# Kernel optimization log

Measured on AMD Instinct MI355X. Metric: run time of the kernel, lower is better.

The kernel has to match this reference:

```python
import jax, jax.numpy as jnp
import numpy as np

BITS = 4
MAXQ = (1 << BITS) - 1  # 15
GROUPSIZE = 128
IN_F = 8192
OUT_F = 8192
PACK = 32 // BITS  # 8 values per int32


def setup_inputs() -> dict:
    key = jax.random.key(0)
    k_x, k_w, k_z, k_s, k_b = jax.random.split(key, 5)
    groups = IN_F // GROUPSIZE
    x = jax.random.normal(k_x, (4, 32, IN_F), dtype=jnp.float32)
    # bit-packed int32 weight / zeros (random bit patterns are valid quantized data)
    qweight = jax.random.randint(k_w, (IN_F // PACK, OUT_F), 0, 2**31 - 1, dtype=jnp.int32)
    qzeros = jax.random.randint(k_z, (groups, OUT_F // PACK), 0, 2**31 - 1, dtype=jnp.int32)
    scales = (jax.random.uniform(k_s, (groups, OUT_F), dtype=jnp.float32) * 0.01 + 1e-3)
    g_idx = (jnp.arange(IN_F, dtype=jnp.int32) // GROUPSIZE).astype(jnp.int32)
    bias = jax.random.normal(k_b, (OUT_F,), dtype=jnp.float32) * 0.01
    return {"x": x, "qweight": qweight, "qzeros": qzeros, "scales": scales,
            "g_idx": g_idx, "bias": bias}


def _dequant(qweight, qzeros, scales, g_idx):
    shifts = jnp.arange(0, 32, BITS, dtype=jnp.int32)  # [PACK]
    # unpack weights along the input dim: [in/PACK, PACK, out] -> [in, out]
    w = (qweight[:, None, :] >> shifts[None, :, None]) & MAXQ
    w = w.reshape(-1, qweight.shape[1])
    # unpack zeros along the output dim: [groups, out/PACK, PACK] -> [groups, out]
    # GPTQ stores (zero - 1), so add 1 back
    z = ((qzeros[:, :, None] >> shifts[None, None, :]) & MAXQ) + 1
    z = z.reshape(qzeros.shape[0], -1)
    # per-group dequant: W[i, o] = scales[g_idx[i], o] * (w[i, o] - z[g_idx[i], o])
    W = scales[g_idx] * (w.astype(scales.dtype) - z[g_idx].astype(scales.dtype))
    return W  # [in, out]


def reference(x, qweight, qzeros, scales, g_idx, bias):
    W = _dequant(qweight, qzeros, scales, g_idx)
    out = jnp.einsum('bsi,io->bso', x, W) + bias
    return out
```

## Files before the change

kernel.cpp:

```cpp
#include <hip/hip_runtime.h>
#include <hip/hip_bf16.h>
#include <stdint.h>


#define IN_F 8192
#define OUT_F 8192
#define MROWS 128
#define KSPLIT 8
#define KCHUNK 1024
#define BM 64

typedef short short8_t __attribute__((ext_vector_type(8)));
typedef float float4_t __attribute__((ext_vector_type(4)));
typedef float float16_t __attribute__((ext_vector_type(16)));

__device__ __forceinline__ void gl_lds16(const void* g, void* l) {
  auto g1 = (const __attribute__((address_space(1))) unsigned int*)((uintptr_t)g);
  auto l3 = (__attribute__((address_space(3))) unsigned int*)((uintptr_t)l);
  __builtin_amdgcn_global_load_lds(g1, l3, 16, 0, 0);
}

__global__ void cvt_x(const float* __restrict__ x, unsigned short* __restrict__ xb) {
  const int i = (blockIdx.x * 256 + threadIdx.x) * 8;
  float4_t a = *(const float4_t*)(x + i);
  float4_t b = *(const float4_t*)(x + i + 4);
  union { short8_t v; __hip_bfloat162 h[4]; } u;
  u.h[0] = __float22bfloat162_rn(make_float2(a.x, a.y));
  u.h[1] = __float22bfloat162_rn(make_float2(a.z, a.w));
  u.h[2] = __float22bfloat162_rn(make_float2(b.x, b.y));
  u.h[3] = __float22bfloat162_rn(make_float2(b.z, b.w));
  *(short8_t*)(xb + i) = u.v;
}

__global__ void reduce_out(const float* __restrict__ part, const float* __restrict__ bias,
                           float* __restrict__ out) {
  const int i = (blockIdx.x * 256 + threadIdx.x) * 4;
  const int o = i & (OUT_F - 1);
  float4_t s = *(const float4_t*)(bias + o);
#pragma unroll
  for (int sl = 0; sl < KSPLIT; ++sl)
    s += *(const float4_t*)(part + (size_t)sl * MROWS * OUT_F + i);
  *(float4_t*)(out + i) = s;
}

__global__ __launch_bounds__(512, 2) void gptq_gemm(
    const unsigned short* __restrict__ xb,
    const int* __restrict__ qweight,
    const int* __restrict__ qzeros,
    const float* __restrict__ scales,
    float* __restrict__ part)
{
  __shared__ unsigned short As[BM * KCHUNK];

  const int tid  = threadIdx.x;
  const int lane = tid & 63;
  const int l31  = lane & 31;
  const int half = lane >> 5;
  const int wv   = tid >> 6;

  const int bid = blockIdx.x;
  const int kb  = bid >> 5;
  const int mb  = (bid >> 4) & 1;
  const int nb  = bid & 15;

  const int kc0 = kb * KCHUNK;
  const int m0  = mb * BM;
  const int g0  = kc0 >> 7;
  const int kp_base = (kc0 >> 3) + half;

  int col[2];
  col[0] = nb * 512 + wv * 64 + l31;
  col[1] = col[0] + 32;

  int   qwc[8][2], qwn[8][2];
  float scc[2], scn[2];
  int   zqc[2], zqn[2];
#pragma unroll
  for (int ks = 0; ks < 8; ++ks)
#pragma unroll
    for (int nt = 0; nt < 2; ++nt)
      qwc[ks][nt] = qweight[(size_t)(kp_base + ks * 2) * OUT_F + col[nt]];
#pragma unroll
  for (int nt = 0; nt < 2; ++nt) {
    scc[nt] = scales[g0 * OUT_F + col[nt]];
    zqc[nt] = qzeros[g0 * (OUT_F / 8) + (col[nt] >> 3)];
  }

  for (int rq = 0; rq < 8; ++rq) {
    const int rl = wv * 8 + rq;
    const unsigned short* grow = xb + (size_t)(m0 + rl) * IN_F + kc0;
#pragma unroll
    for (int hf = 0; hf < 2; ++hf) {
      const int p = hf * 64 + lane;
      const int c = (p & 0x70) | ((p ^ (rl & 15)) & 15);
      gl_lds16(grow + c * 8, (void*)(As + ((size_t)rl * 128 + hf * 64) * 8));
    }
  }
  __syncthreads();

  float16_t acc[2][2];
#pragma unroll
  for (int mt = 0; mt < 2; ++mt)
#pragma unroll
    for (int nt = 0; nt < 2; ++nt)
#pragma unroll
      for (int r = 0; r < 16; ++r) acc[mt][nt][r] = 0.f;

  for (int g = 0; g < 8; ++g) {
    if (g + 1 < 8) {
      const int kp1 = kp_base + (g + 1) * 16;
#pragma unroll
      for (int ks = 0; ks < 8; ++ks)
#pragma unroll
        for (int nt = 0; nt < 2; ++nt)
          qwn[ks][nt] = qweight[(size_t)(kp1 + ks * 2) * OUT_F + col[nt]];
      const int gg = g0 + g + 1;
#pragma unroll
      for (int nt = 0; nt < 2; ++nt) {
        scn[nt] = scales[gg * OUT_F + col[nt]];
        zqn[nt] = qzeros[gg * (OUT_F / 8) + (col[nt] >> 3)];
      }
    }

    float zb[2];
#pragma unroll
    for (int nt = 0; nt < 2; ++nt) {
      const int z = ((zqc[nt] >> (4 * (col[nt] & 7))) & 15) + 1;
      zb[nt] = -scc[nt] * (float)z;
    }

#pragma unroll
    for (int ks = 0; ks < 8; ++ks) {
      const int c = g * 16 + ks * 2 + half;
      const int p = (c & 0x70) | ((c ^ (l31 & 15)) & 15);

      short8_t af[2];
#pragma unroll
      for (int mt = 0; mt < 2; ++mt)
        af[mt] = *(const short8_t*)(As + ((size_t)(mt * 32 + l31) * 128 + p) * 8);

      short8_t bf[2];
#pragma unroll
      for (int nt = 0; nt < 2; ++nt) {
        union { short8_t v; __hip_bfloat162 h[4]; } bw;
        const unsigned q  = (unsigned)qwc[ks][nt];
        const unsigned qe = q & 0x0F0F0F0Fu;
        const unsigned qo = (q >> 4) & 0x0F0F0F0Fu;
#pragma unroll
        for (int jj = 0; jj < 4; ++jj) {
          const float f0 = (float)((qe >> (8 * jj)) & 0xffu);
          const float f1 = (float)((qo >> (8 * jj)) & 0xffu);
          bw.h[jj] = __float22bfloat162_rn(make_float2(
              fmaf(scc[nt], f0, zb[nt]), fmaf(scc[nt], f1, zb[nt])));
        }
        bf[nt] = bw.v;
      }

#pragma unroll
      for (int mt = 0; mt < 2; ++mt)
#pragma unroll
        for (int nt = 0; nt < 2; ++nt)
          acc[mt][nt] = __builtin_amdgcn_mfma_f32_32x32x16_bf16(
              af[mt], bf[nt], acc[mt][nt], 0, 0, 0);
    }

    if (g + 1 < 8) {
#pragma unroll
      for (int ks = 0; ks < 8; ++ks) {
        qwc[ks][0] = qwn[ks][0]; qwc[ks][1] = qwn[ks][1];
      }
      scc[0] = scn[0]; scc[1] = scn[1];
      zqc[0] = zqn[0]; zqc[1] = zqn[1];
    }
  }

  float* base = part + (size_t)kb * (MROWS * OUT_F);
#pragma unroll
  for (int mt = 0; mt < 2; ++mt)
#pragma unroll
    for (int nt = 0; nt < 2; ++nt)
#pragma unroll
      for (int r = 0; r < 16; ++r) {
        const int row = (r & 3) + 8 * (r >> 2) + 4 * half;
        base[(size_t)(m0 + mt * 32 + row) * OUT_F + col[nt]] = acc[mt][nt][r];
      }
}

extern "C" void kernel_launch(void* const* d_in, const int* in_sizes, int n_in,
                              void* d_out, int out_size, void* d_ws, size_t ws_size,
                              hipStream_t stream) {
  const float* x        = (const float*)d_in[0];
  const int*   qweight  = (const int*)d_in[1];
  const int*   qzeros   = (const int*)d_in[2];
  const float* scales   = (const float*)d_in[3];
  const float* bias     = (const float*)d_in[5];
  float* out = (float*)d_out;

  unsigned short* xb = (unsigned short*)d_ws;
  float* part = (float*)((char*)d_ws + (size_t)2 * 1024 * 1024);

  cvt_x<<<dim3((MROWS * IN_F) / (256 * 8)), 256, 0, stream>>>(x, xb);
  gptq_gemm<<<dim3(256), 512, 0, stream>>>(xb, qweight, qzeros, scales, part);
  reduce_out<<<dim3((MROWS * OUT_F) / (256 * 4)), 256, 0, stream>>>(part, bias, out);
}
```

Measured before the change: 116.8 us.

## Fuse x bf16 conversion into GEMM staging and deepen weight prefetch to three buffers

Drops the separate cvt_x kernel: the GEMM loads fp32 activations directly, converts them to bf16 in registers and writes them into the swizzled LDS tile. This removes one launch and the bf16 round trip through global memory, at the cost of twice the global read bytes for x per block and synchronous loads in place of async global_load_lds. The packed weight, scale and zero prefetch also becomes a fully unrolled triple-buffer with distance two, which hides more latency but raises register pressure under launch_bounds(512,2).

```diff
diff --git a/kernel.cpp b/kernel.cpp
--- a/kernel.cpp
+++ b/kernel.cpp
@@ -14,24 +14,6 @@
 typedef float float4_t __attribute__((ext_vector_type(4)));
 typedef float float16_t __attribute__((ext_vector_type(16)));
 
-__device__ __forceinline__ void gl_lds16(const void* g, void* l) {
-  auto g1 = (const __attribute__((address_space(1))) unsigned int*)((uintptr_t)g);
-  auto l3 = (__attribute__((address_space(3))) unsigned int*)((uintptr_t)l);
-  __builtin_amdgcn_global_load_lds(g1, l3, 16, 0, 0);
-}
-
-__global__ void cvt_x(const float* __restrict__ x, unsigned short* __restrict__ xb) {
-  const int i = (blockIdx.x * 256 + threadIdx.x) * 8;
-  float4_t a = *(const float4_t*)(x + i);
-  float4_t b = *(const float4_t*)(x + i + 4);
-  union { short8_t v; __hip_bfloat162 h[4]; } u;
-  u.h[0] = __float22bfloat162_rn(make_float2(a.x, a.y));
-  u.h[1] = __float22bfloat162_rn(make_float2(a.z, a.w));
-  u.h[2] = __float22bfloat162_rn(make_float2(b.x, b.y));
-  u.h[3] = __float22bfloat162_rn(make_float2(b.z, b.w));
-  *(short8_t*)(xb + i) = u.v;
-}
-
 __global__ void reduce_out(const float* __restrict__ part, const float* __restrict__ bias,
                            float* __restrict__ out) {
   const int i = (blockIdx.x * 256 + threadIdx.x) * 4;
@@ -44,7 +26,7 @@
 }
 
 __global__ __launch_bounds__(512, 2) void gptq_gemm(
-    const unsigned short* __restrict__ xb,
+    const float* __restrict__ x,
     const int* __restrict__ qweight,
     const int* __restrict__ qzeros,
     const float* __restrict__ scales,
@@ -72,28 +54,43 @@
   col[0] = nb * 512 + wv * 64 + l31;
   col[1] = col[0] + 32;
 
-  int   qwc[8][2], qwn[8][2];
-  float scc[2], scn[2];
-  int   zqc[2], zqn[2];
+  int   qw[3][8][2];
+  float sc[3][2];
+  int   zq[3][2];
+
+  auto prefetch = [&](int gg, int buf) {
+    const int kp = kp_base + gg * 16;
 #pragma unroll
-  for (int ks = 0; ks < 8; ++ks)
+    for (int ks = 0; ks < 8; ++ks)
 #pragma unroll
-    for (int nt = 0; nt < 2; ++nt)
-      qwc[ks][nt] = qweight[(size_t)(kp_base + ks * 2) * OUT_F + col[nt]];
+      for (int nt = 0; nt < 2; ++nt)
+        qw[buf][ks][nt] = qweight[(size_t)(kp + ks * 2) * OUT_F + col[nt]];
+    const int gg_abs = g0 + gg;
 #pragma unroll
-  for (int nt = 0; nt < 2; ++nt) {
-    scc[nt] = scales[g0 * OUT_F + col[nt]];
-    zqc[nt] = qzeros[g0 * (OUT_F / 8) + (col[nt] >> 3)];
-  }
+    for (int nt = 0; nt < 2; ++nt) {
+      sc[buf][nt] = scales[gg_abs * OUT_F + col[nt]];
+      zq[buf][nt] = qzeros[gg_abs * (OUT_F / 8) + (col[nt] >> 3)];
+    }
+  };
+
+  prefetch(0, 0);
+  prefetch(1, 1);
 
   for (int rq = 0; rq < 8; ++rq) {
     const int rl = wv * 8 + rq;
-    const unsigned short* grow = xb + (size_t)(m0 + rl) * IN_F + kc0;
+    const float* grow = x + (size_t)(m0 + rl) * IN_F + kc0;
 #pragma unroll
     for (int hf = 0; hf < 2; ++hf) {
       const int p = hf * 64 + lane;
       const int c = (p & 0x70) | ((p ^ (rl & 15)) & 15);
-      gl_lds16(grow + c * 8, (void*)(As + ((size_t)rl * 128 + hf * 64) * 8));
+      float4_t a = *(const float4_t*)(grow + c * 8);
+      float4_t b = *(const float4_t*)(grow + c * 8 + 4);
+      union { short8_t v; __hip_bfloat162 h[4]; } u;
+      u.h[0] = __float22bfloat162_rn(make_float2(a.x, a.y));
+      u.h[1] = __float22bfloat162_rn(make_float2(a.z, a.w));
+      u.h[2] = __float22bfloat162_rn(make_float2(b.x, b.y));
+      u.h[3] = __float22bfloat162_rn(make_float2(b.z, b.w));
+      *(short8_t*)(As + ((size_t)rl * 128 + p) * 8) = u.v;
     }
   }
   __syncthreads();
@@ -106,27 +103,17 @@
 #pragma unroll
       for (int r = 0; r < 16; ++r) acc[mt][nt][r] = 0.f;
 
+#pragma unroll
   for (int g = 0; g < 8; ++g) {
-    if (g + 1 < 8) {
-      const int kp1 = kp_base + (g + 1) * 16;
-#pragma unroll
-      for (int ks = 0; ks < 8; ++ks)
-#pragma unroll
-        for (int nt = 0; nt < 2; ++nt)
-          qwn[ks][nt] = qweight[(size_t)(kp1 + ks * 2) * OUT_F + col[nt]];
-      const int gg = g0 + g + 1;
-#pragma unroll
-      for (int nt = 0; nt < 2; ++nt) {
-        scn[nt] = scales[gg * OUT_F + col[nt]];
-        zqn[nt] = qzeros[gg * (OUT_F / 8) + (col[nt] >> 3)];
-      }
-    }
+    const int cur = g % 3;
+
+    if (g + 2 < 8) prefetch(g + 2, (g + 2) % 3);
 
     float zb[2];
 #pragma unroll
     for (int nt = 0; nt < 2; ++nt) {
-      const int z = ((zqc[nt] >> (4 * (col[nt] & 7))) & 15) + 1;
-      zb[nt] = -scc[nt] * (float)z;
+      const int z = ((zq[cur][nt] >> (4 * (col[nt] & 7))) & 15) + 1;
+      zb[nt] = -sc[cur][nt] * (float)z;
     }
 
 #pragma unroll
@@ -143,7 +130,7 @@
 #pragma unroll
       for (int nt = 0; nt < 2; ++nt) {
         union { short8_t v; __hip_bfloat162 h[4]; } bw;
-        const unsigned q  = (unsigned)qwc[ks][nt];
+        const unsigned q  = (unsigned)qw[cur][ks][nt];
         const unsigned qe = q & 0x0F0F0F0Fu;
         const unsigned qo = (q >> 4) & 0x0F0F0F0Fu;
 #pragma unroll
@@ -151,7 +138,7 @@
           const float f0 = (float)((qe >> (8 * jj)) & 0xffu);
           const float f1 = (float)((qo >> (8 * jj)) & 0xffu);
           bw.h[jj] = __float22bfloat162_rn(make_float2(
-              fmaf(scc[nt], f0, zb[nt]), fmaf(scc[nt], f1, zb[nt])));
+              fmaf(sc[cur][nt], f0, zb[nt]), fmaf(sc[cur][nt], f1, zb[nt])));
         }
         bf[nt] = bw.v;
       }
@@ -162,15 +149,6 @@
         for (int nt = 0; nt < 2; ++nt)
           acc[mt][nt] = __builtin_amdgcn_mfma_f32_32x32x16_bf16(
               af[mt], bf[nt], acc[mt][nt], 0, 0, 0);
-    }
-
-    if (g + 1 < 8) {
-#pragma unroll
-      for (int ks = 0; ks < 8; ++ks) {
-        qwc[ks][0] = qwn[ks][0]; qwc[ks][1] = qwn[ks][1];
-      }
-      scc[0] = scn[0]; scc[1] = scn[1];
-      zqc[0] = zqn[0]; zqc[1] = zqn[1];
     }
   }
 
@@ -196,10 +174,8 @@
   const float* bias     = (const float*)d_in[5];
   float* out = (float*)d_out;
 
-  unsigned short* xb = (unsigned short*)d_ws;
-  float* part = (float*)((char*)d_ws + (size_t)2 * 1024 * 1024);
+  float* part = (float*)d_ws;
 
-  cvt_x<<<dim3((MROWS * IN_F) / (256 * 8)), 256, 0, stream>>>(x, xb);
-  gptq_gemm<<<dim3(256), 512, 0, stream>>>(xb, qweight, qzeros, scales, part);
+  gptq_gemm<<<dim3(256), 512, 0, stream>>>(x, qweight, qzeros, scales, part);
   reduce_out<<<dim3((MROWS * OUT_F) / (256 * 4)), 256, 0, stream>>>(part, bias, out);
 }
```

Result: no change. 116.5 us (-0.3%).
